# Optimization experiments

Measured on AMD Instinct MI355X. Metric: run time of the kernel, lower is better.

The kernel has to match this reference:

```python
import jax, jax.numpy as jnp
import numpy as np

H, D = 12, 64  # num_heads, head_dim (embed_size=768)


def setup_inputs() -> dict:
    key = jax.random.key(0)
    k1, k2, k3 = jax.random.split(key, 3)
    z = jax.random.normal(k1, (2, 2048, 768), dtype=jnp.float32)
    W = jax.random.normal(k2, (768, 3 * H * D), dtype=jnp.float32) * (768 ** -0.5)
    bias = jax.random.normal(k3, (3 * H * D,), dtype=jnp.float32) * 0.02
    return {"z": z, "W": W, "bias": bias}


def reference(z, W, bias):
    b, n, _ = z.shape
    # fused QKV projection, reshaped exactly as torch: (b, n, h, d, 3)
    kvq = (z @ W + bias).reshape(b, n, H, D, 3)
    k = kvq[..., 0]  # (b, n, h, d)
    v = kvq[..., 1]
    q = kvq[..., 2]
    qk = jnp.einsum("bqhd,bkhd->bhqk", q, k)  # full O(n^2) scores
    # NOTE: original module scales AFTER softmax (faithful reproduction of bug)
    a = jax.nn.softmax(qk, axis=-1) * (D ** -0.5)
    sa = jnp.einsum("bhqk,bkhd->bqhd", a, v)
    return sa.reshape(b, n, H * D)
```

## Files before the change

### kernel.cpp

```cpp
#include <hip/hip_runtime.h>
#include <hip/hip_bf16.h>
#include <math.h>

#define BB 2
#define NN 2048
#define HH 12
#define DD 64
#define EE 768
#define FF 2304

typedef __attribute__((ext_vector_type(8))) _Float16 f16x8;
typedef __attribute__((ext_vector_type(4))) short bf16x4;
typedef __attribute__((ext_vector_type(4))) float f32x4;
typedef __attribute__((address_space(3))) unsigned int lds_u32;
typedef const __attribute__((address_space(1))) unsigned int glb_u32;

static __device__ __forceinline__ ushort f2bf(float x) {
    __hip_bfloat16 h = __float2bfloat16(x);
    return *reinterpret_cast<ushort*>(&h);
}

__global__ __launch_bounds__(256) void convert_zw(
    const float* __restrict__ z, const float* __restrict__ W,
    _Float16* __restrict__ Zf, _Float16* __restrict__ Wtf)
{
    __shared__ float T[64][65];
    const int t = threadIdx.x;
    if (blockIdx.x < 1536) {
        const int i = (blockIdx.x * 256 + t) * 8;
        const float4 a = *(const float4*)&z[i];
        const float4 b = *(const float4*)&z[i + 4];
        const float v[8] = {a.x, a.y, a.z, a.w, b.x, b.y, b.z, b.w};
        f16x8 h8;
#pragma unroll
        for (int j = 0; j < 8; ++j) h8[j] = (_Float16)v[j];
        *(f16x8*)&Zf[i] = h8;
    } else {
        const int r  = blockIdx.x - 1536;
        const int c0 = (r % 36) * 64;
        const int k0 = (r / 36) * 64;
#pragma unroll
        for (int i = 0; i < 4; ++i) {
            const int row = i * 16 + (t >> 4);
            const int c4  = (t & 15) * 4;
            const float4 w4 = *(const float4*)&W[(size_t)(k0 + row) * FF + c0 + c4];
            T[row][c4 + 0] = w4.x; T[row][c4 + 1] = w4.y;
            T[row][c4 + 2] = w4.z; T[row][c4 + 3] = w4.w;
        }
        __syncthreads();
#pragma unroll
        for (int u = 0; u < 2; ++u) {
            const int id = t + u * 256;
            const int c  = id >> 3;
            const int kc = id & 7;
            f16x8 h8;
#pragma unroll
            for (int j = 0; j < 8; ++j) h8[j] = (_Float16)T[kc * 8 + j][c];
            *(f16x8*)&Wtf[(size_t)(c0 + c) * EE + k0 + kc * 8] = h8;
        }
    }
}

__global__ __launch_bounds__(256, 2) void qkv_gemm(
    const _Float16* __restrict__ Zf, const _Float16* __restrict__ Wtf,
    const float* __restrict__ bias,
    _Float16* __restrict__ Qf, _Float16* __restrict__ Kp,
    ushort* __restrict__ Vp)
{
    __shared__ __align__(16) _Float16 As[128 * 64];
    __shared__ __align__(16) _Float16 Bs[128 * 64];

    const int tid  = threadIdx.x;
    const int wave = tid >> 6;
    const int lane = tid & 63;
    const int l4   = lane & 15;
    const int quad = lane >> 4;
    const int wx   = wave & 1;
    const int wy   = wave >> 1;
    const int row0 = blockIdx.y * 128;
    const int col0 = blockIdx.x * 128;

    int offAB[4], ldsoff[4];
#pragma unroll
    for (int u = 0; u < 4; ++u) {
        const int g = tid + u * 256;
        offAB[u]  = (g >> 3) * EE + (g & 7) * 8;
        ldsoff[u] = (u * 256 + wave * 64) * 16;
    }
    const _Float16* ZB = Zf  + (size_t)row0 * EE;
    const _Float16* WB = Wtf + (size_t)col0 * EE;

    f32x4 acc[4][4];
#pragma unroll
    for (int mi = 0; mi < 4; ++mi)
#pragma unroll
        for (int ni = 0; ni < 4; ++ni) acc[mi][ni] = (f32x4){0.f, 0.f, 0.f, 0.f};

    for (int k0 = 0; k0 < EE; k0 += 64) {
#pragma unroll
        for (int u = 0; u < 4; ++u) {
            __builtin_amdgcn_global_load_lds((glb_u32*)(ZB + offAB[u] + k0),
                                             (lds_u32*)((char*)As + ldsoff[u]), 16, 0, 0);
            __builtin_amdgcn_global_load_lds((glb_u32*)(WB + offAB[u] + k0),
                                             (lds_u32*)((char*)Bs + ldsoff[u]), 16, 0, 0);
        }
        __syncthreads();

#pragma unroll
        for (int ks = 0; ks < 2; ++ks) {
            f16x8 aF[4], bF[4];
#pragma unroll
            for (int mi = 0; mi < 4; ++mi)
                aF[mi] = *(const f16x8*)&As[(wy * 64 + mi * 16 + l4) * 64 + ks * 32 + quad * 8];
#pragma unroll
            for (int ni = 0; ni < 4; ++ni)
                bF[ni] = *(const f16x8*)&Bs[(wx * 64 + ni * 16 + l4) * 64 + ks * 32 + quad * 8];
#pragma unroll
            for (int mi = 0; mi < 4; ++mi)
#pragma unroll
                for (int ni = 0; ni < 4; ++ni)
                    acc[mi][ni] = __builtin_amdgcn_mfma_f32_16x16x32_f16(
                        aF[mi], bF[ni], acc[mi][ni], 0, 0, 0);
        }
        __syncthreads();
    }

#pragma unroll
    for (int ni = 0; ni < 4; ++ni) {
        const int col = col0 + wx * 64 + ni * 16 + l4;
        const int h   = col / 192;
        const int rem = col - h * 192;
        const int d   = rem / 3;
        const int t3  = rem - d * 3;
        const float bv = bias[col];
#pragma unroll
        for (int mi = 0; mi < 4; ++mi) {
#pragma unroll
            for (int r = 0; r < 4; ++r) {
                const int grow = row0 + wy * 64 + mi * 16 + quad * 4 + r;
                const int bb = grow >> 11;
                const int q  = grow & 2047;
                const int bh = bb * HH + h;
                const float val = acc[mi][ni][r] + bv;
                const int s  = q >> 4;
                const int ko = q & 15;
                if (t3 == 0) {
                    const int dc = d >> 5, dd = d & 31;
                    Kp[(size_t)bh * 131072 + s * 1024 + dc * 512 +
                       ((dd >> 3) * 16 + ko) * 8 + (dd & 7)] = (_Float16)val;
                } else if (t3 == 1) {
                    const int dt = d >> 4, l4d = d & 15;
                    Vp[(size_t)bh * 131072 + s * 1024 + dt * 256 +
                       ((ko >> 2) * 16 + l4d) * 4 + (ko & 3)] = f2bf(val);
                } else {
                    Qf[((size_t)bh * NN + q) * DD + d] = (_Float16)(val * 1.44269504f);
                }
            }
        }
    }
}

__global__ __launch_bounds__(256, 3) void attn_kernel(
    const _Float16* __restrict__ Kp, const ushort* __restrict__ Vp,
    const _Float16* __restrict__ Qf, float* __restrict__ out)
{
    __shared__ __align__(16) float Red[3 * 16 * 64 * 4];
    __shared__ float lRed[3][4][16];

    const int tid  = threadIdx.x;
    const int wave = tid >> 6;
    const int lane = tid & 63;
    const int l4   = lane & 15;
    const int quad = lane >> 4;
    const int bh   = blockIdx.x;
    const int q0   = blockIdx.y * 64;

    const _Float16* QB = Qf + (size_t)bh * NN * DD;

    f16x8 qF[4][2];
#pragma unroll
    for (int qc = 0; qc < 4; ++qc) {
        const _Float16* qb = QB + (size_t)(q0 + qc * 16 + l4) * DD + quad * 8;
        qF[qc][0] = *(const f16x8*)qb;
        qF[qc][1] = *(const f16x8*)(qb + 32);
    }

    f32x4 O[4][4];
#pragma unroll
    for (int dt = 0; dt < 4; ++dt)
#pragma unroll
        for (int qc = 0; qc < 4; ++qc) O[dt][qc] = (f32x4){0.f, 0.f, 0.f, 0.f};
    f32x4 lC[4];
#pragma unroll
    for (int qc = 0; qc < 4; ++qc) lC[qc] = (f32x4){0.f, 0.f, 0.f, 0.f};
    const bf16x4 onesA = {(short)0x3F80, (short)0x3F80, (short)0x3F80, (short)0x3F80};

    const _Float16* kp = Kp + (size_t)bh * 131072 + wave * 1024 + lane * 8;
    const ushort*   vp = Vp + (size_t)bh * 131072 + wave * 1024 + lane * 4;

    const f16x8 kA0 = *(const f16x8*)kp;
    const f16x8 kA1 = *(const f16x8*)(kp + 512);
    bf16x4 vF[4];
#pragma unroll
    for (int dt = 0; dt < 4; ++dt)
        vF[dt] = *(const bf16x4*)(vp + dt * 256);
    f16x8 kB0 = *(const f16x8*)(kp + 4096);
    f16x8 kB1 = *(const f16x8*)(kp + 4096 + 512);

    f32x4 sS[4];
#pragma unroll
    for (int qc = 0; qc < 4; ++qc) {
        f32x4 s = {0.f, 0.f, 0.f, 0.f};
        s = __builtin_amdgcn_mfma_f32_16x16x32_f16(kA0, qF[qc][0], s, 0, 0, 0);
        s = __builtin_amdgcn_mfma_f32_16x16x32_f16(kA1, qF[qc][1], s, 0, 0, 0);
        sS[qc] = s;
    }

    for (int it = 0; it < 32; ++it) {
        f16x8 kN0, kN1;
        bf16x4 vN[4];
        if (it < 30) {
            const _Float16* kpn = kp + (it + 2) * 4096;
            kN0 = *(const f16x8*)kpn;
            kN1 = *(const f16x8*)(kpn + 512);
        }
        if (it < 31) {
            const ushort* vpn = vp + (it + 1) * 4096;
#pragma unroll
            for (int dt = 0; dt < 4; ++dt)
                vN[dt] = *(const bf16x4*)(vpn + dt * 256);
        }

        f32x4 sN[4];
        if (it < 31) {
#pragma unroll
            for (int qc = 0; qc < 4; ++qc) {
                f32x4 s = {0.f, 0.f, 0.f, 0.f};
                s = __builtin_amdgcn_mfma_f32_16x16x32_f16(kB0, qF[qc][0], s, 0, 0, 0);
                s = __builtin_amdgcn_mfma_f32_16x16x32_f16(kB1, qF[qc][1], s, 0, 0, 0);
                sN[qc] = s;
            }
        }

        bf16x4 pF[4];
#pragma unroll
        for (int qc = 0; qc < 4; ++qc)
#pragma unroll
            for (int r = 0; r < 4; ++r)
                pF[qc][r] = (short)f2bf(__builtin_amdgcn_exp2f(sS[qc][r]));

#pragma unroll
        for (int qc = 0; qc < 4; ++qc) {
#pragma unroll
            for (int dt = 0; dt < 4; ++dt)
                O[dt][qc] = __builtin_amdgcn_mfma_f32_16x16x16bf16_1k(
                    vF[dt], pF[qc], O[dt][qc], 0, 0, 0);
            lC[qc] = __builtin_amdgcn_mfma_f32_16x16x16bf16_1k(
                onesA, pF[qc], lC[qc], 0, 0, 0);
        }

        if (it < 31) {
#pragma unroll
            for (int qc = 0; qc < 4; ++qc) sS[qc] = sN[qc];
#pragma unroll
            for (int dt = 0; dt < 4; ++dt) vF[dt] = vN[dt];
        }
        if (it < 30) { kB0 = kN0; kB1 = kN1; }
    }

    f32x4* RedV = (f32x4*)Red;
    if (wave > 0) {
        const int wb = (wave - 1) * 16 * 64;
#pragma unroll
        for (int dt = 0; dt < 4; ++dt)
#pragma unroll
            for (int qc = 0; qc < 4; ++qc)
                RedV[wb + (dt * 4 + qc) * 64 + lane] = O[dt][qc];
        if (lane < 16) {
#pragma unroll
            for (int qc = 0; qc < 4; ++qc) lRed[wave - 1][qc][l4] = lC[qc][0];
        }
    }
    __syncthreads();
    if (wave == 0) {
        const int bb = bh / HH;
        const int h  = bh - bb * HH;
        float inv[4];
#pragma unroll
        for (int qc = 0; qc < 4; ++qc)
            inv[qc] = 0.125f /
                (lC[qc][0] + lRed[0][qc][l4] + lRed[1][qc][l4] + lRed[2][qc][l4]);
#pragma unroll
        for (int dt = 0; dt < 4; ++dt) {
#pragma unroll
            for (int qc = 0; qc < 4; ++qc) {
                f32x4 o = O[dt][qc];
#pragma unroll
                for (int w = 0; w < 3; ++w) {
                    const f32x4 o2 = RedV[w * 16 * 64 + (dt * 4 + qc) * 64 + lane];
                    o[0] += o2[0]; o[1] += o2[1]; o[2] += o2[2]; o[3] += o2[3];
                }
                const int q = q0 + qc * 16 + l4;
                float4 ov;
                ov.x = o[0] * inv[qc]; ov.y = o[1] * inv[qc];
                ov.z = o[2] * inv[qc]; ov.w = o[3] * inv[qc];
                *(float4*)&out[((size_t)(bb * NN + q)) * (HH * DD) + h * DD +
                               dt * 16 + quad * 4] = ov;
            }
        }
    }
}

extern "C" void kernel_launch(void* const* d_in, const int* in_sizes, int n_in,
                              void* d_out, int out_size, void* d_ws, size_t ws_size,
                              hipStream_t stream)
{
    const float* z    = (const float*)d_in[0];
    const float* W    = (const float*)d_in[1];
    const float* bias = (const float*)d_in[2];
    float* out = (float*)d_out;

    const size_t N1 = (size_t)BB * HH * NN * DD;
    const size_t NW = (size_t)EE * FF;
    _Float16* ws  = (_Float16*)d_ws;
    _Float16* Zf  = ws;
    _Float16* Wtf = ws + N1;
    _Float16* Qf  = ws + N1 + NW;
    _Float16* Kp  = ws + 2 * N1 + NW;
    ushort*   Vp  = (ushort*)(ws + 3 * N1 + NW);

    convert_zw<<<dim3(1968), 256, 0, stream>>>(z, W, Zf, Wtf);
    qkv_gemm<<<dim3(18, 32), 256, 0, stream>>>(Zf, Wtf, bias, Qf, Kp, Vp);
    attn_kernel<<<dim3(24, 32), 256, 0, stream>>>(Kp, Vp, Qf, out);
}
```

Baseline: 144.2 us.

## Permute W columns by Q/K/V, swizzle GEMM LDS, vectorize packed epilogue stores

After: 134.1 us. 7.0% less time.

```diff
diff --git a/kernel.cpp b/kernel.cpp
--- a/kernel.cpp
+++ b/kernel.cpp
@@ -18,6 +18,12 @@
 static __device__ __forceinline__ ushort f2bf(float x) {
     __hip_bfloat16 h = __float2bfloat16(x);
     return *reinterpret_cast<ushort*>(&h);
+}
+static __device__ __forceinline__ ushort f2h(float x) {
+    _Float16 h = (_Float16)x;
+    ushort u;
+    __builtin_memcpy(&u, &h, 2);
+    return u;
 }
 
 __global__ __launch_bounds__(256) void convert_zw(
@@ -50,13 +56,19 @@
         __syncthreads();
 #pragma unroll
         for (int u = 0; u < 2; ++u) {
-            const int id = t + u * 256;
-            const int c  = id >> 3;
-            const int kc = id & 7;
+            const int id  = t + u * 256;
+            const int c   = id >> 3;
+            const int kc  = id & 7;
+            const int col = c0 + c;
+            const int h   = col / 192;
+            const int rem = col - h * 192;
+            const int d   = rem / 3;
+            const int t3  = rem - d * 3;
+            const int cp  = t3 * 768 + h * 64 + d;
             f16x8 h8;
 #pragma unroll
             for (int j = 0; j < 8; ++j) h8[j] = (_Float16)T[kc * 8 + j][c];
-            *(f16x8*)&Wtf[(size_t)(c0 + c) * EE + k0 + kc * 8] = h8;
+            *(f16x8*)&Wtf[(size_t)cp * EE + k0 + kc * 8] = h8;
         }
     }
 }
@@ -64,7 +76,7 @@
 __global__ __launch_bounds__(256, 2) void qkv_gemm(
     const _Float16* __restrict__ Zf, const _Float16* __restrict__ Wtf,
     const float* __restrict__ bias,
-    _Float16* __restrict__ Qf, _Float16* __restrict__ Kp,
+    _Float16* __restrict__ Qp, _Float16* __restrict__ Kp,
     ushort* __restrict__ Vp)
 {
     __shared__ __align__(16) _Float16 As[128 * 64];
@@ -79,12 +91,13 @@
     const int wy   = wave >> 1;
     const int row0 = blockIdx.y * 128;
     const int col0 = blockIdx.x * 128;
+    const int tq   = blockIdx.x / 6;
 
     int offAB[4], ldsoff[4];
 #pragma unroll
     for (int u = 0; u < 4; ++u) {
         const int g = tid + u * 256;
-        offAB[u]  = (g >> 3) * EE + (g & 7) * 8;
+        offAB[u]  = (g >> 3) * EE + (((g & 7) ^ ((g >> 3) & 7)) * 8);
         ldsoff[u] = (u * 256 + wave * 64) * 16;
     }
     const _Float16* ZB = Zf  + (size_t)row0 * EE;
@@ -110,51 +123,91 @@
         for (int ks = 0; ks < 2; ++ks) {
             f16x8 aF[4], bF[4];
 #pragma unroll
-            for (int mi = 0; mi < 4; ++mi)
-                aF[mi] = *(const f16x8*)&As[(wy * 64 + mi * 16 + l4) * 64 + ks * 32 + quad * 8];
-#pragma unroll
-            for (int ni = 0; ni < 4; ++ni)
-                bF[ni] = *(const f16x8*)&Bs[(wx * 64 + ni * 16 + l4) * 64 + ks * 32 + quad * 8];
-#pragma unroll
-            for (int mi = 0; mi < 4; ++mi)
-#pragma unroll
-                for (int ni = 0; ni < 4; ++ni)
-                    acc[mi][ni] = __builtin_amdgcn_mfma_f32_16x16x32_f16(
-                        aF[mi], bF[ni], acc[mi][ni], 0, 0, 0);
+            for (int mi = 0; mi < 4; ++mi) {
+                const int rA = wy * 64 + mi * 16 + l4;
+                aF[mi] = *(const f16x8*)&As[rA * 64 + (((ks * 4 + quad) ^ (rA & 7)) * 8)];
+            }
+#pragma unroll
+            for (int ni = 0; ni < 4; ++ni) {
+                const int rB = wx * 64 + ni * 16 + l4;
+                bF[ni] = *(const f16x8*)&Bs[rB * 64 + (((ks * 4 + quad) ^ (rB & 7)) * 8)];
+            }
+            if (tq == 1) {
+#pragma unroll
+                for (int mi = 0; mi < 4; ++mi)
+#pragma unroll
+                    for (int ni = 0; ni < 4; ++ni)
+                        acc[mi][ni] = __builtin_amdgcn_mfma_f32_16x16x32_f16(
+                            aF[mi], bF[ni], acc[mi][ni], 0, 0, 0);
+            } else {
+#pragma unroll
+                for (int mi = 0; mi < 4; ++mi)
+#pragma unroll
+                    for (int ni = 0; ni < 4; ++ni)
+                        acc[mi][ni] = __builtin_amdgcn_mfma_f32_16x16x32_f16(
+                            bF[ni], aF[mi], acc[mi][ni], 0, 0, 0);
+            }
         }
         __syncthreads();
     }
 
-#pragma unroll
-    for (int ni = 0; ni < 4; ++ni) {
-        const int col = col0 + wx * 64 + ni * 16 + l4;
-        const int h   = col / 192;
-        const int rem = col - h * 192;
-        const int d   = rem / 3;
-        const int t3  = rem - d * 3;
-        const float bv = bias[col];
-#pragma unroll
-        for (int mi = 0; mi < 4; ++mi) {
-#pragma unroll
-            for (int r = 0; r < 4; ++r) {
-                const int grow = row0 + wy * 64 + mi * 16 + quad * 4 + r;
+    if (tq == 1) {
+#pragma unroll
+        for (int ni = 0; ni < 4; ++ni) {
+            const int cv = col0 + wx * 64 + ni * 16 + l4 - 768;
+            const int h  = cv >> 6;
+            const int d  = cv & 63;
+            const int dt = d >> 4, ld = d & 15;
+            const float bv = bias[h * 192 + d * 3 + 1];
+#pragma unroll
+            for (int mi = 0; mi < 4; ++mi) {
+                const int grow = row0 + wy * 64 + mi * 16 + quad * 4;
                 const int bb = grow >> 11;
-                const int q  = grow & 2047;
-                const int bh = bb * HH + h;
-                const float val = acc[mi][ni][r] + bv;
-                const int s  = q >> 4;
-                const int ko = q & 15;
-                if (t3 == 0) {
-                    const int dc = d >> 5, dd = d & 31;
-                    Kp[(size_t)bh * 131072 + s * 1024 + dc * 512 +
-                       ((dd >> 3) * 16 + ko) * 8 + (dd & 7)] = (_Float16)val;
-                } else if (t3 == 1) {
-                    const int dt = d >> 4, l4d = d & 15;
-                    Vp[(size_t)bh * 131072 + s * 1024 + dt * 256 +
-                       ((ko >> 2) * 16 + l4d) * 4 + (ko & 3)] = f2bf(val);
+                const int qq = grow & 2047;
+                const int s  = qq >> 4;
+                ushort4 st;
+                st.x = f2bf(acc[mi][ni][0] + bv);
+                st.y = f2bf(acc[mi][ni][1] + bv);
+                st.z = f2bf(acc[mi][ni][2] + bv);
+                st.w = f2bf(acc[mi][ni][3] + bv);
+                *(ushort4*)&Vp[(size_t)(bb * HH + h) * 131072 + s * 1024 +
+                               dt * 256 + (quad * 16 + ld) * 4] = st;
+            }
+        }
+    } else {
+        const bool isQ = (tq == 2);
+        ushort* dstP = (ushort*)(isQ ? Qp : Kp);
+#pragma unroll
+        for (int ni = 0; ni < 4; ++ni) {
+            const int cp  = col0 + wx * 64 + ni * 16 + quad * 4 - (isQ ? 1536 : 0);
+            const int h   = cp >> 6;
+            const int d0  = cp & 63;
+            const int dc  = d0 >> 5;
+            const int dd0 = d0 & 31;
+            const int t3  = isQ ? 2 : 0;
+            float bvs[4];
+#pragma unroll
+            for (int r = 0; r < 4; ++r) bvs[r] = bias[h * 192 + (d0 + r) * 3 + t3];
+#pragma unroll
+            for (int mi = 0; mi < 4; ++mi) {
+                const int grow = row0 + wy * 64 + mi * 16 + l4;
+                const int bb = grow >> 11;
+                const int qq = grow & 2047;
+                const int s  = qq >> 4;
+                ushort4 st;
+                if (isQ) {
+                    st.x = f2h((acc[mi][ni][0] + bvs[0]) * 1.44269504f);
+                    st.y = f2h((acc[mi][ni][1] + bvs[1]) * 1.44269504f);
+                    st.z = f2h((acc[mi][ni][2] + bvs[2]) * 1.44269504f);
+                    st.w = f2h((acc[mi][ni][3] + bvs[3]) * 1.44269504f);
                 } else {
-                    Qf[((size_t)bh * NN + q) * DD + d] = (_Float16)(val * 1.44269504f);
+                    st.x = f2h(acc[mi][ni][0] + bvs[0]);
+                    st.y = f2h(acc[mi][ni][1] + bvs[1]);
+                    st.z = f2h(acc[mi][ni][2] + bvs[2]);
+                    st.w = f2h(acc[mi][ni][3] + bvs[3]);
                 }
+                *(ushort4*)&dstP[(size_t)(bb * HH + h) * 131072 + s * 1024 +
+                                 dc * 512 + ((dd0 >> 3) * 16 + l4) * 8 + (dd0 & 7)] = st;
             }
         }
     }
@@ -162,7 +215,7 @@
 
 __global__ __launch_bounds__(256, 3) void attn_kernel(
     const _Float16* __restrict__ Kp, const ushort* __restrict__ Vp,
-    const _Float16* __restrict__ Qf, float* __restrict__ out)
+    const _Float16* __restrict__ Qp, float* __restrict__ out)
 {
     __shared__ __align__(16) float Red[3 * 16 * 64 * 4];
     __shared__ float lRed[3][4][16];
@@ -175,14 +228,13 @@
     const int bh   = blockIdx.x;
     const int q0   = blockIdx.y * 64;
 
-    const _Float16* QB = Qf + (size_t)bh * NN * DD;
-
     f16x8 qF[4][2];
 #pragma unroll
     for (int qc = 0; qc < 4; ++qc) {
-        const _Float16* qb = QB + (size_t)(q0 + qc * 16 + l4) * DD + quad * 8;
+        const _Float16* qb = Qp + (size_t)bh * 131072 +
+                             (blockIdx.y * 4 + qc) * 1024 + lane * 8;
         qF[qc][0] = *(const f16x8*)qb;
-        qF[qc][1] = *(const f16x8*)(qb + 32);
+        qF[qc][1] = *(const f16x8*)(qb + 512);
     }
 
     f32x4 O[4][4];
@@ -325,11 +377,11 @@
     _Float16* ws  = (_Float16*)d_ws;
     _Float16* Zf  = ws;
     _Float16* Wtf = ws + N1;
-    _Float16* Qf  = ws + N1 + NW;
+    _Float16* Qp  = ws + N1 + NW;
     _Float16* Kp  = ws + 2 * N1 + NW;
     ushort*   Vp  = (ushort*)(ws + 3 * N1 + NW);
 
     convert_zw<<<dim3(1968), 256, 0, stream>>>(z, W, Zf, Wtf);
-    qkv_gemm<<<dim3(18, 32), 256, 0, stream>>>(Zf, Wtf, bias, Qf, Kp, Vp);
-    attn_kernel<<<dim3(24, 32), 256, 0, stream>>>(Kp, Vp, Qf, out);
-}
+    qkv_gemm<<<dim3(18, 32), 256, 0, stream>>>(Zf, Wtf, bias, Qp, Kp, Vp);
+    attn_kernel<<<dim3(24, 32), 256, 0, stream>>>(Kp, Vp, Qp, out);
+}
```
